# Kernel optimization log

Hardware: AMD Instinct MI355X
Metric: run time of the kernel (lower is better)

Reference implementation:

```python
import jax, jax.numpy as jnp
import numpy as np

NUM_VIEWS = 11

def setup_inputs() -> dict:
    key = jax.random.key(0)
    ks = jax.random.split(key, 6)
    BF, T, D_IN, D_OUT, R = 128, 196, 1024, 1024, 4
    B = 16
    x = jax.random.normal(ks[0], (BF, T, D_IN), dtype=jnp.float32)
    view_idx = jax.random.randint(ks[1], (B,), 0, NUM_VIEWS)
    W = jax.random.normal(ks[2], (D_OUT, D_IN), dtype=jnp.float32) * (1.0 / np.sqrt(D_IN))
    b = jax.random.normal(ks[3], (D_OUT,), dtype=jnp.float32) * 0.01
    lora_A = jax.random.normal(ks[4], (NUM_VIEWS, D_IN, R), dtype=jnp.float32) * (1.0 / np.sqrt(D_IN))
    lora_B = jax.random.normal(ks[5], (NUM_VIEWS, R, D_OUT), dtype=jnp.float32) * 0.02
    return {"x": x, "view_idx": view_idx, "W": W, "b": b, "lora_A": lora_A, "lora_B": lora_B}

def reference(x, view_idx, W, b, lora_A, lora_B):
    # base linear: [BF, T, D_in] @ [D_in, D_out]
    out = jnp.einsum('bti,oi->bto', x, W) + b
    BF = x.shape[0]
    B = view_idx.shape[0]
    if BF != B:  # static shapes -> Python branch is jit-safe
        curr = jnp.repeat(view_idx, BF // B)  # expand per-frame view index
    else:
        curr = view_idx
    curr = jnp.clip(curr, 0, NUM_VIEWS - 1)
    A = lora_A[curr]          # [BF, D_in, R] gathered per sample
    Bm = lora_B[curr]         # [BF, R, D_out]
    h = jnp.einsum('bti,bir->btr', x, A)      # low-rank projection
    lora = jnp.einsum('btr,bro->bto', h, Bm)  # back to D_out
    return out + lora
```

## Files before the change

kernel.cpp:

```cpp
#include <hip/hip_runtime.h>
#include <hip/hip_bf16.h>
#include <stdint.h>

#define M_TOT 25088
#define N_TOT 1024
#define K_TOT 1024
#define T_LEN 196
#define NVIEW 11

#define BM 128
#define BN 128
#define BK 64

typedef unsigned short u16;
typedef __bf16 bf16x8 __attribute__((ext_vector_type(8)));
typedef float f32x4 __attribute__((ext_vector_type(4)));
typedef unsigned short u16x4 __attribute__((ext_vector_type(4)));

#define XB_ELEMS (M_TOT * (size_t)K_TOT)
#define WB_ELEMS (N_TOT * (size_t)K_TOT)
#define WB_OFF_B (XB_ELEMS * 2)
#define H_OFF_B  (WB_OFF_B + WB_ELEMS * 2)
#define WS_NEEDED (H_OFF_B + (size_t)M_TOT * 4 * 4)

__device__ __forceinline__ u16 f2bf(float f) {
    union { float f; unsigned int i; } c; c.f = f;
    unsigned int i = c.i;
    return (u16)((i + 0x7FFFu + ((i >> 16) & 1u)) >> 16);
}

__global__ __launch_bounds__(256) void convert_h_kernel(
    const float* __restrict__ x, const float* __restrict__ W,
    const int* __restrict__ view_idx, const float* __restrict__ lora_A,
    u16* __restrict__ xb, u16* __restrict__ wb, float* __restrict__ h) {
    const int wave = threadIdx.x >> 6;
    const int lane = threadIdx.x & 63;
    const int blk  = blockIdx.x;

    if (blk >= M_TOT / 4) {
        const int row = (blk - M_TOT / 4) * 4 + wave;
        const float* src = W + (size_t)row * K_TOT;
        u16* dst = wb + (size_t)row * K_TOT;
#pragma unroll
        for (int it = 0; it < 4; ++it) {
            const int k = it * 256 + lane * 4;
            float4 v = *(const float4*)(src + k);
            u16x4 o = { f2bf(v.x), f2bf(v.y), f2bf(v.z), f2bf(v.w) };
            *(u16x4*)(dst + k) = o;
        }
        return;
    }

    const int row = blk * 4 + wave;
    const int bf  = row / T_LEN;
    int v = view_idx[bf >> 3];
    v = v < 0 ? 0 : (v > NVIEW - 1 ? NVIEW - 1 : v);
    const float* A  = lora_A + (size_t)v * (K_TOT * 4);
    const float* xr = x + (size_t)row * K_TOT;
    u16* dst = xb + (size_t)row * K_TOT;

    float a0 = 0.f, a1 = 0.f, a2 = 0.f, a3 = 0.f;
#pragma unroll
    for (int it = 0; it < 4; ++it) {
        const int k = it * 256 + lane * 4;
        float4 xv = *(const float4*)(xr + k);
        u16x4 o = { f2bf(xv.x), f2bf(xv.y), f2bf(xv.z), f2bf(xv.w) };
        *(u16x4*)(dst + k) = o;
        const float xf[4] = { xv.x, xv.y, xv.z, xv.w };
#pragma unroll
        for (int j = 0; j < 4; ++j) {
            float4 av = *(const float4*)(A + (size_t)(k + j) * 4);
            a0 += xf[j] * av.x; a1 += xf[j] * av.y;
            a2 += xf[j] * av.z; a3 += xf[j] * av.w;
        }
    }
#pragma unroll
    for (int off = 32; off > 0; off >>= 1) {
        a0 += __shfl_xor(a0, off, 64);
        a1 += __shfl_xor(a1, off, 64);
        a2 += __shfl_xor(a2, off, 64);
        a3 += __shfl_xor(a3, off, 64);
    }
    if (lane == 0)
        *(float4*)(h + (size_t)row * 4) = make_float4(a0, a1, a2, a3);
}

__global__ __launch_bounds__(256) void h_only_kernel(
    const float* __restrict__ x, const int* __restrict__ view_idx,
    const float* __restrict__ lora_A, float* __restrict__ h) {
    const int row  = blockIdx.x * 4 + (threadIdx.x >> 6);
    const int lane = threadIdx.x & 63;
    int v = view_idx[(row / T_LEN) >> 3];
    v = v < 0 ? 0 : (v > NVIEW - 1 ? NVIEW - 1 : v);
    const float* A  = lora_A + (size_t)v * (K_TOT * 4);
    const float* xr = x + (size_t)row * K_TOT;
    float a0 = 0.f, a1 = 0.f, a2 = 0.f, a3 = 0.f;
#pragma unroll
    for (int it = 0; it < 4; ++it) {
        const int k = it * 256 + lane * 4;
        float4 xv = *(const float4*)(xr + k);
        const float xf[4] = { xv.x, xv.y, xv.z, xv.w };
#pragma unroll
        for (int j = 0; j < 4; ++j) {
            float4 av = *(const float4*)(A + (size_t)(k + j) * 4);
            a0 += xf[j] * av.x; a1 += xf[j] * av.y;
            a2 += xf[j] * av.z; a3 += xf[j] * av.w;
        }
    }
#pragma unroll
    for (int off = 32; off > 0; off >>= 1) {
        a0 += __shfl_xor(a0, off, 64);
        a1 += __shfl_xor(a1, off, 64);
        a2 += __shfl_xor(a2, off, 64);
        a3 += __shfl_xor(a3, off, 64);
    }
    if (lane == 0)
        *(float4*)(h + (size_t)row * 4) = make_float4(a0, a1, a2, a3);
}

template <bool CONV>
__global__ __launch_bounds__(256) void gemm_lora_kernel(
    const void* __restrict__ xp, const void* __restrict__ Wp,
    const float* __restrict__ bias, const int* __restrict__ view_idx,
    const float* __restrict__ lora_B, const float* __restrict__ h,
    float* __restrict__ out) {
    __shared__ u16 As[BM * BK];
    __shared__ u16 Bs[BN * BK];

    const int tid  = threadIdx.x;
    const int bx   = blockIdx.x;
    const int by   = blockIdx.y;
    const int lane = tid & 63;
    const int wave = tid >> 6;
    const int wm   = (wave >> 1) * 64;
    const int wn   = (wave & 1) * 64;
    const int l16  = lane & 15;
    const int quad = lane >> 4;

    const size_t a_base = (size_t)(by * BM) * K_TOT;
    const size_t b_base = (size_t)(bx * BN) * K_TOT;

    f32x4 acc[4][4] = {};

    for (int kt = 0; kt < K_TOT / BK; ++kt) {
        const int kofs = kt * BK;
        if constexpr (!CONV) {
            const u16* x = (const u16*)xp;
            const u16* W = (const u16*)Wp;
#pragma unroll
            for (int i = 0; i < 4; ++i) {
                const int e = i * 2048 + tid * 8;
                const int r = e >> 6, c = e & 63;
                __builtin_amdgcn_global_load_lds(
                    (const __attribute__((address_space(1))) void*)(x + a_base + (size_t)r * K_TOT + kofs + c),
                    (__attribute__((address_space(3))) void*)(As + e), 16, 0, 0);
                __builtin_amdgcn_global_load_lds(
                    (const __attribute__((address_space(1))) void*)(W + b_base + (size_t)r * K_TOT + kofs + c),
                    (__attribute__((address_space(3))) void*)(Bs + e), 16, 0, 0);
            }
        } else {
            const float* x = (const float*)xp;
            const float* W = (const float*)Wp;
#pragma unroll
            for (int i = 0; i < 8; ++i) {
                const int e = i * 1024 + tid * 4;
                const int r = e >> 6, c = e & 63;
                float4 av = *(const float4*)(x + a_base + (size_t)r * K_TOT + kofs + c);
                float4 bv = *(const float4*)(W + b_base + (size_t)r * K_TOT + kofs + c);
                u16x4 ao = { f2bf(av.x), f2bf(av.y), f2bf(av.z), f2bf(av.w) };
                u16x4 bo = { f2bf(bv.x), f2bf(bv.y), f2bf(bv.z), f2bf(bv.w) };
                *(u16x4*)(As + e) = ao;
                *(u16x4*)(Bs + e) = bo;
            }
        }
        __syncthreads();
#pragma unroll
        for (int kk = 0; kk < 2; ++kk) {
            const int k0 = kk * 32 + quad * 8;
            bf16x8 a_frag[4], b_frag[4];
#pragma unroll
            for (int mi = 0; mi < 4; ++mi)
                a_frag[mi] = *(const bf16x8*)(const void*)(As + (wm + mi * 16 + l16) * BK + k0);
#pragma unroll
            for (int ni = 0; ni < 4; ++ni)
                b_frag[ni] = *(const bf16x8*)(const void*)(Bs + (wn + ni * 16 + l16) * BK + k0);
#pragma unroll
            for (int mi = 0; mi < 4; ++mi)
#pragma unroll
                for (int ni = 0; ni < 4; ++ni)
                    acc[mi][ni] = __builtin_amdgcn_mfma_f32_16x16x32_bf16(
                        a_frag[mi], b_frag[ni], acc[mi][ni], 0, 0, 0);
        }
        __syncthreads();
    }

    const int rowBase = by * BM + wm;
    const int colBase = bx * BN + wn;
    float biasv[4];
#pragma unroll
    for (int ni = 0; ni < 4; ++ni) biasv[ni] = bias[colBase + ni * 16 + l16];

#pragma unroll
    for (int mi = 0; mi < 4; ++mi) {
#pragma unroll
        for (int reg = 0; reg < 4; ++reg) {
            const int grow = rowBase + mi * 16 + quad * 4 + reg;
            int v = view_idx[(grow / T_LEN) >> 3];
            v = v < 0 ? 0 : (v > NVIEW - 1 ? NVIEW - 1 : v);
            const float4 hv = *(const float4*)(h + (size_t)grow * 4);
            const float* Bv = lora_B + (size_t)v * (4 * N_TOT);
            float* orow = out + (size_t)grow * N_TOT;
#pragma unroll
            for (int ni = 0; ni < 4; ++ni) {
                const int gcol = colBase + ni * 16 + l16;
                float lora = hv.x * Bv[gcol]
                           + hv.y * Bv[N_TOT + gcol]
                           + hv.z * Bv[2 * N_TOT + gcol]
                           + hv.w * Bv[3 * N_TOT + gcol];
                orow[gcol] = acc[mi][ni][reg] + biasv[ni] + lora;
            }
        }
    }
}

extern "C" void kernel_launch(void* const* d_in, const int* in_sizes, int n_in,
                              void* d_out, int out_size, void* d_ws, size_t ws_size,
                              hipStream_t stream) {
    const float* x        = (const float*)d_in[0];
    const int*   view_idx = (const int*)d_in[1];
    const float* W        = (const float*)d_in[2];
    const float* b        = (const float*)d_in[3];
    const float* lora_A   = (const float*)d_in[4];
    const float* lora_B   = (const float*)d_in[5];
    float* out = (float*)d_out;

    const dim3 ggrid(N_TOT / BN, M_TOT / BM);
    if (ws_size >= WS_NEEDED) {
        u16*   xb = (u16*)d_ws;
        u16*   wb = (u16*)((char*)d_ws + WB_OFF_B);
        float* h  = (float*)((char*)d_ws + H_OFF_B);
        hipLaunchKernelGGL(convert_h_kernel, dim3(M_TOT / 4 + N_TOT / 4), dim3(256), 0, stream,
                           x, W, view_idx, lora_A, xb, wb, h);
        hipLaunchKernelGGL((gemm_lora_kernel<false>), ggrid, dim3(256), 0, stream,
                           xb, wb, b, view_idx, lora_B, h, out);
    } else {
        float* h = (float*)d_ws;
        hipLaunchKernelGGL(h_only_kernel, dim3(M_TOT / 4), dim3(256), 0, stream,
                           x, view_idx, lora_A, h);
        hipLaunchKernelGGL((gemm_lora_kernel<true>), ggrid, dim3(256), 0, stream,
                           x, W, b, view_idx, lora_B, h, out);
    }
}
```

Measured before the change: 299.2 us.

## Split cast and LoRA projection kernels, swizzle GEMM tile order, hoist lora_B loads

```diff
diff --git a/kernel.cpp b/kernel.cpp
--- a/kernel.cpp
+++ b/kernel.cpp
@@ -7,6 +7,7 @@
 #define K_TOT 1024
 #define T_LEN 196
 #define NVIEW 11
+#define ROWS_PER_VIEW 1568
 
 #define BM 128
 #define BN 128
@@ -15,10 +16,10 @@
 typedef unsigned short u16;
 typedef __bf16 bf16x8 __attribute__((ext_vector_type(8)));
 typedef float f32x4 __attribute__((ext_vector_type(4)));
-typedef unsigned short u16x4 __attribute__((ext_vector_type(4)));
-
-#define XB_ELEMS (M_TOT * (size_t)K_TOT)
-#define WB_ELEMS (N_TOT * (size_t)K_TOT)
+typedef unsigned short u16x8 __attribute__((ext_vector_type(8)));
+
+#define XB_ELEMS ((size_t)M_TOT * K_TOT)
+#define WB_ELEMS ((size_t)N_TOT * K_TOT)
 #define WB_OFF_B (XB_ELEMS * 2)
 #define H_OFF_B  (WB_OFF_B + WB_ELEMS * 2)
 #define WS_NEEDED (H_OFF_B + (size_t)M_TOT * 4 * 4)
@@ -28,51 +29,48 @@
     unsigned int i = c.i;
     return (u16)((i + 0x7FFFu + ((i >> 16) & 1u)) >> 16);
 }
-
-__global__ __launch_bounds__(256) void convert_h_kernel(
+__device__ __forceinline__ float bf2f(unsigned int u) {
+    union { unsigned int i; float f; } c; c.i = u << 16; return c.f;
+}
+
+__global__ __launch_bounds__(256) void cast_kernel(
     const float* __restrict__ x, const float* __restrict__ W,
-    const int* __restrict__ view_idx, const float* __restrict__ lora_A,
-    u16* __restrict__ xb, u16* __restrict__ wb, float* __restrict__ h) {
-    const int wave = threadIdx.x >> 6;
+    u16* __restrict__ xb, u16* __restrict__ wb) {
+    const size_t e = ((size_t)blockIdx.x * 256 + threadIdx.x) * 8;
+    const float* src;
+    u16* dst;
+    if (e < XB_ELEMS) { src = x + e; dst = xb + e; }
+    else              { src = W + (e - XB_ELEMS); dst = wb + (e - XB_ELEMS); }
+    float4 v0 = *(const float4*)src;
+    float4 v1 = *(const float4*)(src + 4);
+    u16x8 o = { f2bf(v0.x), f2bf(v0.y), f2bf(v0.z), f2bf(v0.w),
+                f2bf(v1.x), f2bf(v1.y), f2bf(v1.z), f2bf(v1.w) };
+    *(u16x8*)dst = o;
+}
+
+__global__ __launch_bounds__(256) void h_kernel(
+    const u16* __restrict__ xb, const int* __restrict__ view_idx,
+    const float* __restrict__ lora_A, float* __restrict__ h) {
+    const int row  = blockIdx.x * 4 + (threadIdx.x >> 6);
     const int lane = threadIdx.x & 63;
-    const int blk  = blockIdx.x;
-
-    if (blk >= M_TOT / 4) {
-        const int row = (blk - M_TOT / 4) * 4 + wave;
-        const float* src = W + (size_t)row * K_TOT;
-        u16* dst = wb + (size_t)row * K_TOT;
-#pragma unroll
-        for (int it = 0; it < 4; ++it) {
-            const int k = it * 256 + lane * 4;
-            float4 v = *(const float4*)(src + k);
-            u16x4 o = { f2bf(v.x), f2bf(v.y), f2bf(v.z), f2bf(v.w) };
-            *(u16x4*)(dst + k) = o;
-        }
-        return;
-    }
-
-    const int row = blk * 4 + wave;
-    const int bf  = row / T_LEN;
-    int v = view_idx[bf >> 3];
+    int v = view_idx[row / ROWS_PER_VIEW];
     v = v < 0 ? 0 : (v > NVIEW - 1 ? NVIEW - 1 : v);
-    const float* A  = lora_A + (size_t)v * (K_TOT * 4);
-    const float* xr = x + (size_t)row * K_TOT;
-    u16* dst = xb + (size_t)row * K_TOT;
+    const float* A = lora_A + (size_t)v * (K_TOT * 4);
+    const unsigned int* xr = (const unsigned int*)(xb + (size_t)row * K_TOT);
 
     float a0 = 0.f, a1 = 0.f, a2 = 0.f, a3 = 0.f;
 #pragma unroll
-    for (int it = 0; it < 4; ++it) {
-        const int k = it * 256 + lane * 4;
-        float4 xv = *(const float4*)(xr + k);
-        u16x4 o = { f2bf(xv.x), f2bf(xv.y), f2bf(xv.z), f2bf(xv.w) };
-        *(u16x4*)(dst + k) = o;
-        const float xf[4] = { xv.x, xv.y, xv.z, xv.w };
-#pragma unroll
-        for (int j = 0; j < 4; ++j) {
-            float4 av = *(const float4*)(A + (size_t)(k + j) * 4);
-            a0 += xf[j] * av.x; a1 += xf[j] * av.y;
-            a2 += xf[j] * av.z; a3 += xf[j] * av.w;
-        }
+    for (int it = 0; it < 8; ++it) {
+        unsigned int p = xr[it * 64 + lane];
+        float x0 = bf2f(p & 0xffffu);
+        float x1 = bf2f(p >> 16);
+        const int k = it * 128 + lane * 2;
+        float4 av0 = *(const float4*)(A + (size_t)k * 4);
+        float4 av1 = *(const float4*)(A + (size_t)k * 4 + 4);
+        a0 += x0 * av0.x + x1 * av1.x;
+        a1 += x0 * av0.y + x1 * av1.y;
+        a2 += x0 * av0.z + x1 * av1.z;
+        a3 += x0 * av0.w + x1 * av1.w;
     }
 #pragma unroll
     for (int off = 32; off > 0; off >>= 1) {
@@ -90,22 +88,17 @@
     const float* __restrict__ lora_A, float* __restrict__ h) {
     const int row  = blockIdx.x * 4 + (threadIdx.x >> 6);
     const int lane = threadIdx.x & 63;
-    int v = view_idx[(row / T_LEN) >> 3];
+    int v = view_idx[row / ROWS_PER_VIEW];
     v = v < 0 ? 0 : (v > NVIEW - 1 ? NVIEW - 1 : v);
     const float* A  = lora_A + (size_t)v * (K_TOT * 4);
     const float* xr = x + (size_t)row * K_TOT;
     float a0 = 0.f, a1 = 0.f, a2 = 0.f, a3 = 0.f;
 #pragma unroll
-    for (int it = 0; it < 4; ++it) {
-        const int k = it * 256 + lane * 4;
-        float4 xv = *(const float4*)(xr + k);
-        const float xf[4] = { xv.x, xv.y, xv.z, xv.w };
-#pragma unroll
-        for (int j = 0; j < 4; ++j) {
-            float4 av = *(const float4*)(A + (size_t)(k + j) * 4);
-            a0 += xf[j] * av.x; a1 += xf[j] * av.y;
-            a2 += xf[j] * av.z; a3 += xf[j] * av.w;
-        }
+    for (int it = 0; it < 16; ++it) {
+        const int k = it * 64 + lane;
+        float xf = xr[k];
+        float4 av = *(const float4*)(A + (size_t)k * 4);
+        a0 += xf * av.x; a1 += xf * av.y; a2 += xf * av.z; a3 += xf * av.w;
     }
 #pragma unroll
     for (int off = 32; off > 0; off >>= 1) {
@@ -127,9 +120,12 @@
     __shared__ u16 As[BM * BK];
     __shared__ u16 Bs[BN * BK];
 
-    const int tid  = threadIdx.x;
-    const int bx   = blockIdx.x;
-    const int by   = blockIdx.y;
+    const int tid = threadIdx.x;
+    const int id = blockIdx.x;
+    int bx, by;
+    if (id < 1536) { const int c = id >> 6, w = id & 63; by = c * 8 + (w & 7); bx = w >> 3; }
+    else           { const int r = id - 1536; by = 192 + (r & 3); bx = r >> 2; }
+
     const int lane = tid & 63;
     const int wave = tid >> 6;
     const int wm   = (wave >> 1) * 64;
@@ -167,10 +163,10 @@
                 const int r = e >> 6, c = e & 63;
                 float4 av = *(const float4*)(x + a_base + (size_t)r * K_TOT + kofs + c);
                 float4 bv = *(const float4*)(W + b_base + (size_t)r * K_TOT + kofs + c);
-                u16x4 ao = { f2bf(av.x), f2bf(av.y), f2bf(av.z), f2bf(av.w) };
-                u16x4 bo = { f2bf(bv.x), f2bf(bv.y), f2bf(bv.z), f2bf(bv.w) };
-                *(u16x4*)(As + e) = ao;
-                *(u16x4*)(Bs + e) = bo;
+                *(u16*)(As + e)     = f2bf(av.x); *(u16*)(As + e + 1) = f2bf(av.y);
+                *(u16*)(As + e + 2) = f2bf(av.z); *(u16*)(As + e + 3) = f2bf(av.w);
+                *(u16*)(Bs + e)     = f2bf(bv.x); *(u16*)(Bs + e + 1) = f2bf(bv.y);
+                *(u16*)(Bs + e + 2) = f2bf(bv.z); *(u16*)(Bs + e + 3) = f2bf(bv.w);
             }
         }
         __syncthreads();
@@ -200,24 +196,53 @@
 #pragma unroll
     for (int ni = 0; ni < 4; ++ni) biasv[ni] = bias[colBase + ni * 16 + l16];
 
-#pragma unroll
-    for (int mi = 0; mi < 4; ++mi) {
-#pragma unroll
-        for (int reg = 0; reg < 4; ++reg) {
-            const int grow = rowBase + mi * 16 + quad * 4 + reg;
-            int v = view_idx[(grow / T_LEN) >> 3];
-            v = v < 0 ? 0 : (v > NVIEW - 1 ? NVIEW - 1 : v);
-            const float4 hv = *(const float4*)(h + (size_t)grow * 4);
-            const float* Bv = lora_B + (size_t)v * (4 * N_TOT);
-            float* orow = out + (size_t)grow * N_TOT;
-#pragma unroll
-            for (int ni = 0; ni < 4; ++ni) {
-                const int gcol = colBase + ni * 16 + l16;
-                float lora = hv.x * Bv[gcol]
-                           + hv.y * Bv[N_TOT + gcol]
-                           + hv.z * Bv[2 * N_TOT + gcol]
-                           + hv.w * Bv[3 * N_TOT + gcol];
-                orow[gcol] = acc[mi][ni][reg] + biasv[ni] + lora;
+    const int ve0 = (by * BM) / ROWS_PER_VIEW;
+    const int ve1 = (by * BM + BM - 1) / ROWS_PER_VIEW;
+    if (ve0 == ve1) {
+        int v = view_idx[ve0];
+        v = v < 0 ? 0 : (v > NVIEW - 1 ? NVIEW - 1 : v);
+        const float* Bv = lora_B + (size_t)v * (4 * N_TOT);
+        float Bvv[4][4];
+#pragma unroll
+        for (int r = 0; r < 4; ++r)
+#pragma unroll
+            for (int ni = 0; ni < 4; ++ni)
+                Bvv[r][ni] = Bv[r * N_TOT + colBase + ni * 16 + l16];
+#pragma unroll
+        for (int mi = 0; mi < 4; ++mi) {
+#pragma unroll
+            for (int reg = 0; reg < 4; ++reg) {
+                const int grow = rowBase + mi * 16 + quad * 4 + reg;
+                const float4 hv = *(const float4*)(h + (size_t)grow * 4);
+                float* orow = out + (size_t)grow * N_TOT;
+#pragma unroll
+                for (int ni = 0; ni < 4; ++ni) {
+                    float lora = hv.x * Bvv[0][ni] + hv.y * Bvv[1][ni]
+                               + hv.z * Bvv[2][ni] + hv.w * Bvv[3][ni];
+                    orow[colBase + ni * 16 + l16] = acc[mi][ni][reg] + biasv[ni] + lora;
+                }
+            }
+        }
+    } else {
+#pragma unroll
+        for (int mi = 0; mi < 4; ++mi) {
+#pragma unroll
+            for (int reg = 0; reg < 4; ++reg) {
+                const int grow = rowBase + mi * 16 + quad * 4 + reg;
+                int v = view_idx[grow / ROWS_PER_VIEW];
+                v = v < 0 ? 0 : (v > NVIEW - 1 ? NVIEW - 1 : v);
+                const float4 hv = *(const float4*)(h + (size_t)grow * 4);
+                const float* Bv = lora_B + (size_t)v * (4 * N_TOT);
+                float* orow = out + (size_t)grow * N_TOT;
+#pragma unroll
+                for (int ni = 0; ni < 4; ++ni) {
+                    const int gcol = colBase + ni * 16 + l16;
+                    float lora = hv.x * Bv[gcol]
+                               + hv.y * Bv[N_TOT + gcol]
+                               + hv.z * Bv[2 * N_TOT + gcol]
+                               + hv.w * Bv[3 * N_TOT + gcol];
+                    orow[gcol] = acc[mi][ni][reg] + biasv[ni] + lora;
+                }
             }
         }
     }
@@ -234,13 +259,14 @@
     const float* lora_B   = (const float*)d_in[5];
     float* out = (float*)d_out;
 
-    const dim3 ggrid(N_TOT / BN, M_TOT / BM);
+    const dim3 ggrid((M_TOT / BM) * (N_TOT / BN));
     if (ws_size >= WS_NEEDED) {
         u16*   xb = (u16*)d_ws;
         u16*   wb = (u16*)((char*)d_ws + WB_OFF_B);
         float* h  = (float*)((char*)d_ws + H_OFF_B);
-        hipLaunchKernelGGL(convert_h_kernel, dim3(M_TOT / 4 + N_TOT / 4), dim3(256), 0, stream,
-                           x, W, view_idx, lora_A, xb, wb, h);
+        const int cast_blocks = (int)((XB_ELEMS + WB_ELEMS) / (8 * 256));
+        hipLaunchKernelGGL(cast_kernel, dim3(cast_blocks), dim3(256), 0, stream, x, W, xb, wb);
+        hipLaunchKernelGGL(h_kernel, dim3(M_TOT / 4), dim3(256), 0, stream, xb, view_idx, lora_A, h);
         hipLaunchKernelGGL((gemm_lora_kernel<false>), ggrid, dim3(256), 0, stream,
                            xb, wb, b, view_idx, lora_B, h, out);
     } else {
```

Result: no change. 304.4 us (+1.7%).
